# Optimization experiments

Measured on AMD Instinct MI355X. Metric: run time of the kernel, lower is better.

Reference implementation:

```python
import jax, jax.numpy as jnp
import numpy as np

EMA_DECAY = 0.9

K, B, D, d = 16, 2048, 1024, 64


def setup_inputs() -> dict:
    key = jax.random.key(0)
    k1, k2 = jax.random.split(key)
    x = jax.random.normal(k1, (B, D), dtype=jnp.float32)
    # subspace bases, scaled like orthonormal-ish columns
    Us = jax.random.normal(k2, (K, D, d), dtype=jnp.float32) / np.sqrt(D)
    c_mean = jnp.ones((K,), dtype=jnp.float32) / K
    return {"x": x, "Us": Us, "c_mean": c_mean}


def reference(x, Us, c_mean):
    # encode: per-subspace projection coefficients z = Us^T x  -> (k, B, d)
    z = jnp.einsum("bD,kDd->kbd", x, Us)
    # decode: x_ = z @ Us^T  -> (k, B, D)
    x_ = jnp.einsum("kbd,kDd->kbD", z, Us)
    # per-(sample, subspace) squared reconstruction loss -> (B, k)
    losses = jnp.sum((x[None, :, :] - x_) ** 2, axis=2).T
    # hard assignment: one-hot of argmin over subspaces (detached in original)
    assign_obj = jax.lax.stop_gradient(losses)
    minidx = jnp.argmin(assign_obj, axis=1)  # (B,)
    c = jax.nn.one_hot(minidx, K, dtype=losses.dtype)  # (B, k)
    # EMA cluster-usage statistics
    batch_c_mean = jnp.mean(c, axis=0)  # (k,)
    c_mean_new = EMA_DECAY * c_mean + (1.0 - EMA_DECAY) * batch_c_mean
    # objective: mean over batch of assigned losses, summed over clusters
    loss_k = jnp.mean(c * losses, axis=0)  # (k,)
    obj = jnp.sum(loss_k)
    return x_, c, c_mean_new, obj
```

## Files before the change

kernel.cpp:

```cpp
#include <hip/hip_runtime.h>

#define Kk  16
#define Bb  2048
#define Dd  1024
#define dd_ 64
#define BT  64
#define CH  64
#define PAD 68

__global__ __launch_bounds__(256) void k_xnorm(const float* __restrict__ x,
                                               float* __restrict__ xnorm) {
    int lane = threadIdx.x & 63;
    int w    = threadIdx.x >> 6;
    int b    = blockIdx.x * 4 + w;
    const float* xr = x + (size_t)b * Dd;
    float s = 0.f;
#pragma unroll
    for (int seg = 0; seg < 4; ++seg) {
        float4 v = *reinterpret_cast<const float4*>(xr + seg * 256 + lane * 4);
        s = fmaf(v.x, v.x, s); s = fmaf(v.y, v.y, s);
        s = fmaf(v.z, v.z, s); s = fmaf(v.w, v.w, s);
    }
#pragma unroll
    for (int off = 32; off > 0; off >>= 1) s += __shfl_down(s, off, 64);
    if (lane == 0) xnorm[b] = s;
}

__global__ __launch_bounds__(256) void k_fused(const float* __restrict__ x,
                                               const float* __restrict__ Us,
                                               float* __restrict__ xhat,
                                               float* __restrict__ znorm,
                                               float* __restrict__ hatnorm) {
    __shared__ float buf0[CH][PAD];
    __shared__ float buf1[CH][PAD];
    __shared__ float z_lds[dd_][PAD];
    __shared__ float hat_lds[BT];

    int t  = threadIdx.x;
    int tx = t & 15;
    int ty = t >> 4;

    int bid = blockIdx.x;
    int sw  = (bid & 7) * 64 + (bid >> 3);
    int k   = sw >> 5;
    int b0  = (sw & 31) * BT;

    const float* __restrict__ xk  = x  + (size_t)b0 * Dd;
    const float* __restrict__ Usk = Us + (size_t)k * Dd * dd_;

    if (t < BT) hat_lds[t] = 0.f;

    float acc[4][4];
#pragma unroll
    for (int i = 0; i < 4; ++i)
#pragma unroll
        for (int j = 0; j < 4; ++j) acc[i][j] = 0.f;

    for (int Dc = 0; Dc < Dd; Dc += CH) {
        __syncthreads();
#pragma unroll
        for (int rr = 0; rr < 4; ++rr) {
            int row = rr * 16 + ty;
            float4 v = *reinterpret_cast<const float4*>(
                xk + (size_t)row * Dd + Dc + tx * 4);
            buf0[tx * 4 + 0][row] = v.x;
            buf0[tx * 4 + 1][row] = v.y;
            buf0[tx * 4 + 2][row] = v.z;
            buf0[tx * 4 + 3][row] = v.w;
            float4 u = *reinterpret_cast<const float4*>(
                Usk + (size_t)(Dc + row) * dd_ + tx * 4);
            *reinterpret_cast<float4*>(&buf1[row][tx * 4]) = u;
        }
        __syncthreads();
#pragma unroll 8
        for (int kk = 0; kk < CH; ++kk) {
            float4 av = *reinterpret_cast<const float4*>(&buf0[kk][tx * 4]);
            float4 bv = *reinterpret_cast<const float4*>(&buf1[kk][ty * 4]);
            float a_[4] = {av.x, av.y, av.z, av.w};
            float b_[4] = {bv.x, bv.y, bv.z, bv.w};
#pragma unroll
            for (int i = 0; i < 4; ++i)
#pragma unroll
                for (int j = 0; j < 4; ++j)
                    acc[i][j] = fmaf(a_[i], b_[j], acc[i][j]);
        }
    }

#pragma unroll
    for (int i = 0; i < 4; ++i)
#pragma unroll
        for (int j = 0; j < 4; ++j)
            z_lds[ty * 4 + j][tx * 4 + i] = acc[i][j];
    __syncthreads();

    if (t < BT) {
        float s = 0.f;
#pragma unroll 8
        for (int dc = 0; dc < dd_; ++dc) {
            float zv = z_lds[dc][t];
            s = fmaf(zv, zv, s);
        }
        znorm[k * Bb + b0 + t] = s;
    }

    float hat[4] = {0.f, 0.f, 0.f, 0.f};
    for (int Dc = 0; Dc < Dd; Dc += CH) {
        __syncthreads();
#pragma unroll
        for (int rr = 0; rr < 4; ++rr) {
            int row = rr * 16 + ty;
            float4 u = *reinterpret_cast<const float4*>(
                Usk + (size_t)(Dc + row) * dd_ + tx * 4);
            buf0[tx * 4 + 0][row] = u.x;
            buf0[tx * 4 + 1][row] = u.y;
            buf0[tx * 4 + 2][row] = u.z;
            buf0[tx * 4 + 3][row] = u.w;
        }
        __syncthreads();

        float dacc[4][4];
#pragma unroll
        for (int i = 0; i < 4; ++i)
#pragma unroll
            for (int j = 0; j < 4; ++j) dacc[i][j] = 0.f;

#pragma unroll 8
        for (int kk = 0; kk < dd_; ++kk) {
            float4 av = *reinterpret_cast<const float4*>(&z_lds[kk][ty * 4]);
            float4 bv = *reinterpret_cast<const float4*>(&buf0[kk][tx * 4]);
            float a_[4] = {av.x, av.y, av.z, av.w};
            float b_[4] = {bv.x, bv.y, bv.z, bv.w};
#pragma unroll
            for (int i = 0; i < 4; ++i)
#pragma unroll
                for (int j = 0; j < 4; ++j)
                    dacc[i][j] = fmaf(a_[i], b_[j], dacc[i][j]);
        }

#pragma unroll
        for (int i = 0; i < 4; ++i) {
            float4 o = make_float4(dacc[i][0], dacc[i][1], dacc[i][2], dacc[i][3]);
            *reinterpret_cast<float4*>(
                xhat + ((size_t)(k * Bb + b0 + ty * 4 + i)) * Dd + Dc + tx * 4) = o;
            hat[i] = fmaf(o.x, o.x, hat[i]);
            hat[i] = fmaf(o.y, o.y, hat[i]);
            hat[i] = fmaf(o.z, o.z, hat[i]);
            hat[i] = fmaf(o.w, o.w, hat[i]);
        }
    }

    __syncthreads();
#pragma unroll
    for (int i = 0; i < 4; ++i) atomicAdd(&hat_lds[ty * 4 + i], hat[i]);
    __syncthreads();
    if (t < BT) hatnorm[k * Bb + b0 + t] = hat_lds[t];
}

__global__ __launch_bounds__(128) void k_assign(const float* __restrict__ znorm,
                                                const float* __restrict__ hatnorm,
                                                const float* __restrict__ xnorm,
                                                float* __restrict__ c,
                                                float* __restrict__ cnt_g,
                                                float* __restrict__ obj_g) {
    __shared__ float cnt[Kk];
    __shared__ float objacc;
    int t = threadIdx.x;
    int b = blockIdx.x * 128 + t;
    if (t < Kk) cnt[t] = 0.f;
    if (t == 0) objacc = 0.f;
    __syncthreads();

    float xn   = xnorm[b];
    float best = 3.4e38f;
    int   bi   = 0;
#pragma unroll
    for (int k = 0; k < Kk; ++k) {
        float l = xn - 2.f * znorm[k * Bb + b] + hatnorm[k * Bb + b];
        if (l < best) { best = l; bi = k; }
    }
#pragma unroll
    for (int j = 0; j < 4; ++j) {
        float4 o;
        o.x = (bi == j * 4 + 0) ? 1.f : 0.f;
        o.y = (bi == j * 4 + 1) ? 1.f : 0.f;
        o.z = (bi == j * 4 + 2) ? 1.f : 0.f;
        o.w = (bi == j * 4 + 3) ? 1.f : 0.f;
        *reinterpret_cast<float4*>(&c[(size_t)b * Kk + j * 4]) = o;
    }
    atomicAdd(&cnt[bi], 1.f);

    float lobj = best;
#pragma unroll
    for (int off = 32; off > 0; off >>= 1) lobj += __shfl_down(lobj, off, 64);
    if ((t & 63) == 0) atomicAdd(&objacc, lobj);
    __syncthreads();

    if (t < Kk) atomicAdd(&cnt_g[t], cnt[t]);
    if (t == 0) atomicAdd(obj_g, objacc);
}

__global__ __launch_bounds__(64) void k_epilogue(const float* __restrict__ cnt_g,
                                                 const float* __restrict__ obj_g,
                                                 const float* __restrict__ c_mean,
                                                 float* __restrict__ c_mean_new,
                                                 float* __restrict__ obj) {
    int t = threadIdx.x;
    if (t < Kk) c_mean_new[t] = 0.9f * c_mean[t] + 0.1f * (cnt_g[t] * (1.f / Bb));
    if (t == 0) obj[0] = obj_g[0] * (1.f / Bb);
}

extern "C" void kernel_launch(void* const* d_in, const int* in_sizes, int n_in,
                              void* d_out, int out_size, void* d_ws, size_t ws_size,
                              hipStream_t stream) {
    const float* x      = (const float*)d_in[0];
    const float* Us     = (const float*)d_in[1];
    const float* c_mean = (const float*)d_in[2];

    float* out        = (float*)d_out;
    float* xhat       = out;
    float* c          = out + (size_t)Kk * Bb * Dd;
    float* c_mean_new = c + (size_t)Bb * Kk;
    float* obj        = c_mean_new + Kk;

    float* ws      = (float*)d_ws;
    float* znorm   = ws;
    float* hatnorm = znorm + (size_t)Kk * Bb;
    float* xnorm   = hatnorm + (size_t)Kk * Bb;
    float* cnt_g   = xnorm + Bb;
    float* obj_g   = cnt_g + Kk;

    hipMemsetAsync(cnt_g, 0, (Kk + 1) * sizeof(float), stream);

    k_xnorm   <<<Bb / 4, 256, 0, stream>>>(x, xnorm);
    k_fused   <<<Kk * (Bb / BT), 256, 0, stream>>>(x, Us, xhat, znorm, hatnorm);
    k_assign  <<<Bb / 128, 128, 0, stream>>>(znorm, hatnorm, xnorm, c, cnt_g, obj_g);
    k_epilogue<<<1, 64, 0, stream>>>(cnt_g, obj_g, c_mean, c_mean_new, obj);
}
```

Baseline: 273.9 us.

## Register-prefetch next chunk, XOR-swizzle LDS, fold xnorm into assign, drop memset

The encode and decode loops now load the next chunk from global memory into registers while computing on the current one, then write it to LDS after a barrier. The transposed LDS buffer uses an XOR swizzle instead of padding to avoid bank conflicts. The z-norm is computed from the accumulators with LDS atomics, and only a combined hat-minus-2z term is written out. The separate xnorm kernel and the memset are removed: x norms are computed inside the assign kernel, which now writes per-block partials that a final kernel sums. This cuts launches, but the assign stage now runs on only 8 blocks that each read 256 rows of x serially.

```diff
diff --git a/kernel.cpp b/kernel.cpp
--- a/kernel.cpp
+++ b/kernel.cpp
@@ -6,34 +6,67 @@
 #define dd_ 64
 #define BT  64
 #define CH  64
-#define PAD 68
-
-__global__ __launch_bounds__(256) void k_xnorm(const float* __restrict__ x,
-                                               float* __restrict__ xnorm) {
-    int lane = threadIdx.x & 63;
-    int w    = threadIdx.x >> 6;
-    int b    = blockIdx.x * 4 + w;
-    const float* xr = x + (size_t)b * Dd;
-    float s = 0.f;
-#pragma unroll
-    for (int seg = 0; seg < 4; ++seg) {
-        float4 v = *reinterpret_cast<const float4*>(xr + seg * 256 + lane * 4);
-        s = fmaf(v.x, v.x, s); s = fmaf(v.y, v.y, s);
-        s = fmaf(v.z, v.z, s); s = fmaf(v.w, v.w, s);
-    }
-#pragma unroll
-    for (int off = 32; off > 0; off >>= 1) s += __shfl_down(s, off, 64);
-    if (lane == 0) xnorm[b] = s;
+#define NCH (Dd / CH)
+
+__device__ __forceinline__ int swz(int c) { return ((c >> 2) & 7) << 2; }
+
+__device__ __forceinline__ void enc_load(const float* __restrict__ xk,
+                                         const float* __restrict__ Usk,
+                                         int Dc, int tx, int ty,
+                                         float4 nx[4], float4 nu[4]) {
+#pragma unroll
+    for (int rr = 0; rr < 4; ++rr) {
+        int row = rr * 16 + ty;
+        nx[rr] = *reinterpret_cast<const float4*>(xk + (size_t)row * Dd + Dc + tx * 4);
+        nu[rr] = *reinterpret_cast<const float4*>(Usk + (size_t)(Dc + row) * dd_ + tx * 4);
+    }
+}
+
+__device__ __forceinline__ void enc_store(float (*bufT)[64], float (*bufS)[64],
+                                          int tx, int ty,
+                                          const float4 nx[4], const float4 nu[4]) {
+    int sx = (tx & 7) << 2;
+#pragma unroll
+    for (int rr = 0; rr < 4; ++rr) {
+        int row = rr * 16 + ty;
+        bufT[tx * 4 + 0][row ^ sx] = nx[rr].x;
+        bufT[tx * 4 + 1][row ^ sx] = nx[rr].y;
+        bufT[tx * 4 + 2][row ^ sx] = nx[rr].z;
+        bufT[tx * 4 + 3][row ^ sx] = nx[rr].w;
+        *reinterpret_cast<float4*>(&bufS[row][tx * 4]) = nu[rr];
+    }
+}
+
+__device__ __forceinline__ void dec_load(const float* __restrict__ Usk,
+                                         int Dc, int tx, int ty, float4 nU[4]) {
+#pragma unroll
+    for (int rr = 0; rr < 4; ++rr) {
+        int row = rr * 16 + ty;
+        nU[rr] = *reinterpret_cast<const float4*>(Usk + (size_t)(Dc + row) * dd_ + tx * 4);
+    }
+}
+
+__device__ __forceinline__ void dec_store(float (*bufT)[64], int tx, int ty,
+                                          const float4 nU[4]) {
+    int sx = (tx & 7) << 2;
+#pragma unroll
+    for (int rr = 0; rr < 4; ++rr) {
+        int row = rr * 16 + ty;
+        bufT[tx * 4 + 0][row ^ sx] = nU[rr].x;
+        bufT[tx * 4 + 1][row ^ sx] = nU[rr].y;
+        bufT[tx * 4 + 2][row ^ sx] = nU[rr].z;
+        bufT[tx * 4 + 3][row ^ sx] = nU[rr].w;
+    }
 }
 
 __global__ __launch_bounds__(256) void k_fused(const float* __restrict__ x,
                                                const float* __restrict__ Us,
                                                float* __restrict__ xhat,
-                                               float* __restrict__ znorm,
-                                               float* __restrict__ hatnorm) {
-    __shared__ float buf0[CH][PAD];
-    __shared__ float buf1[CH][PAD];
-    __shared__ float z_lds[dd_][PAD];
+                                               float* __restrict__ lterm) {
+    __shared__ float bufT[CH][64];
+    __shared__ float bufS[CH][64];
+    __shared__ float z_lds[dd_][68];
+    __shared__ float zn_lds[BT];
     __shared__ float hat_lds[BT];
 
     int t  = threadIdx.x;
@@ -48,7 +81,7 @@
     const float* __restrict__ xk  = x  + (size_t)b0 * Dd;
     const float* __restrict__ Usk = Us + (size_t)k * Dd * dd_;
 
-    if (t < BT) hat_lds[t] = 0.f;
+    if (t < BT) { zn_lds[t] = 0.f; hat_lds[t] = 0.f; }
 
     float acc[4][4];
 #pragma unroll
@@ -56,26 +89,19 @@
 #pragma unroll
         for (int j = 0; j < 4; ++j) acc[i][j] = 0.f;
 
-    for (int Dc = 0; Dc < Dd; Dc += CH) {
-        __syncthreads();
-#pragma unroll
-        for (int rr = 0; rr < 4; ++rr) {
-            int row = rr * 16 + ty;
-            float4 v = *reinterpret_cast<const float4*>(
-                xk + (size_t)row * Dd + Dc + tx * 4);
-            buf0[tx * 4 + 0][row] = v.x;
-            buf0[tx * 4 + 1][row] = v.y;
-            buf0[tx * 4 + 2][row] = v.z;
-            buf0[tx * 4 + 3][row] = v.w;
-            float4 u = *reinterpret_cast<const float4*>(
-                Usk + (size_t)(Dc + row) * dd_ + tx * 4);
-            *reinterpret_cast<float4*>(&buf1[row][tx * 4]) = u;
-        }
-        __syncthreads();
+    float4 nx[4], nu[4];
+    enc_load(xk, Usk, 0, tx, ty, nx, nu);
+    enc_store(bufT, bufS, tx, ty, nx, nu);
+    __syncthreads();
+
+    for (int ch = 0; ch < NCH; ++ch) {
+        bool more = (ch + 1 < NCH);
+        if (more) enc_load(xk, Usk, (ch + 1) * CH, tx, ty, nx, nu);
+
 #pragma unroll 8
         for (int kk = 0; kk < CH; ++kk) {
-            float4 av = *reinterpret_cast<const float4*>(&buf0[kk][tx * 4]);
-            float4 bv = *reinterpret_cast<const float4*>(&buf1[kk][ty * 4]);
+            float4 av = *reinterpret_cast<const float4*>(&bufT[kk][(tx * 4) ^ swz(kk)]);
+            float4 bv = *reinterpret_cast<const float4*>(&bufS[kk][ty * 4]);
             float a_[4] = {av.x, av.y, av.z, av.w};
             float b_[4] = {bv.x, bv.y, bv.z, bv.w};
 #pragma unroll
@@ -84,39 +110,32 @@
                 for (int j = 0; j < 4; ++j)
                     acc[i][j] = fmaf(a_[i], b_[j], acc[i][j]);
         }
-    }
-
-#pragma unroll
-    for (int i = 0; i < 4; ++i)
-#pragma unroll
-        for (int j = 0; j < 4; ++j)
+        __syncthreads();
+        if (more) { enc_store(bufT, bufS, tx, ty, nx, nu); __syncthreads(); }
+    }
+
+#pragma unroll
+    for (int i = 0; i < 4; ++i) {
+        float pz = 0.f;
+#pragma unroll
+        for (int j = 0; j < 4; ++j) {
             z_lds[ty * 4 + j][tx * 4 + i] = acc[i][j];
-    __syncthreads();
-
-    if (t < BT) {
-        float s = 0.f;
-#pragma unroll 8
-        for (int dc = 0; dc < dd_; ++dc) {
-            float zv = z_lds[dc][t];
-            s = fmaf(zv, zv, s);
-        }
-        znorm[k * Bb + b0 + t] = s;
-    }
+            pz = fmaf(acc[i][j], acc[i][j], pz);
+        }
+        atomicAdd(&zn_lds[tx * 4 + i], pz);
+    }
+    __syncthreads();
 
     float hat[4] = {0.f, 0.f, 0.f, 0.f};
-    for (int Dc = 0; Dc < Dd; Dc += CH) {
-        __syncthreads();
-#pragma unroll
-        for (int rr = 0; rr < 4; ++rr) {
-            int row = rr * 16 + ty;
-            float4 u = *reinterpret_cast<const float4*>(
-                Usk + (size_t)(Dc + row) * dd_ + tx * 4);
-            buf0[tx * 4 + 0][row] = u.x;
-            buf0[tx * 4 + 1][row] = u.y;
-            buf0[tx * 4 + 2][row] = u.z;
-            buf0[tx * 4 + 3][row] = u.w;
-        }
-        __syncthreads();
+    float4 nU[4];
+    dec_load(Usk, 0, tx, ty, nU);
+    dec_store(bufT, tx, ty, nU);
+    __syncthreads();
+
+    for (int ch = 0; ch < NCH; ++ch) {
+        bool more = (ch + 1 < NCH);
+        int  Dc   = ch * CH;
+        if (more) dec_load(Usk, Dc + CH, tx, ty, nU);
 
         float dacc[4][4];
 #pragma unroll
@@ -127,7 +146,7 @@
 #pragma unroll 8
         for (int kk = 0; kk < dd_; ++kk) {
             float4 av = *reinterpret_cast<const float4*>(&z_lds[kk][ty * 4]);
-            float4 bv = *reinterpret_cast<const float4*>(&buf0[kk][tx * 4]);
+            float4 bv = *reinterpret_cast<const float4*>(&bufT[kk][(tx * 4) ^ swz(kk)]);
             float a_[4] = {av.x, av.y, av.z, av.w};
             float b_[4] = {bv.x, bv.y, bv.z, bv.w};
 #pragma unroll
@@ -141,41 +160,61 @@
         for (int i = 0; i < 4; ++i) {
             float4 o = make_float4(dacc[i][0], dacc[i][1], dacc[i][2], dacc[i][3]);
             *reinterpret_cast<float4*>(
-                xhat + ((size_t)(k * Bb + b0 + ty * 4 + i)) * Dd + Dc + tx * 4) = o;
+                xhat + (size_t)(k * Bb + b0 + ty * 4 + i) * Dd + Dc + tx * 4) = o;
             hat[i] = fmaf(o.x, o.x, hat[i]);
             hat[i] = fmaf(o.y, o.y, hat[i]);
             hat[i] = fmaf(o.z, o.z, hat[i]);
             hat[i] = fmaf(o.w, o.w, hat[i]);
         }
-    }
-
-    __syncthreads();
+        __syncthreads();
+        if (more) { dec_store(bufT, tx, ty, nU); __syncthreads(); }
+    }
+
 #pragma unroll
     for (int i = 0; i < 4; ++i) atomicAdd(&hat_lds[ty * 4 + i], hat[i]);
     __syncthreads();
-    if (t < BT) hatnorm[k * Bb + b0 + t] = hat_lds[t];
-}
-
-__global__ __launch_bounds__(128) void k_assign(const float* __restrict__ znorm,
-                                                const float* __restrict__ hatnorm,
-                                                const float* __restrict__ xnorm,
+    if (t < BT) lterm[k * Bb + b0 + t] = hat_lds[t] - 2.f * zn_lds[t];
+}
+
+__global__ __launch_bounds__(256) void k_assign(const float* __restrict__ x,
+                                                const float* __restrict__ lterm,
                                                 float* __restrict__ c,
-                                                float* __restrict__ cnt_g,
-                                                float* __restrict__ obj_g) {
+                                                float* __restrict__ cnt_part,
+                                                float* __restrict__ obj_part) {
+    __shared__ float xn_lds[256];
     __shared__ float cnt[Kk];
     __shared__ float objacc;
-    int t = threadIdx.x;
-    int b = blockIdx.x * 128 + t;
+    int t    = threadIdx.x;
+    int lane = t & 63;
+    int w    = t >> 6;
+    int bbase = blockIdx.x * 256;
+
     if (t < Kk) cnt[t] = 0.f;
     if (t == 0) objacc = 0.f;
-    __syncthreads();
-
-    float xn   = xnorm[b];
+
+    for (int r = 0; r < 64; ++r) {
+        int bl = w * 64 + r;
+        const float* xr = x + (size_t)(bbase + bl) * Dd;
+        float s = 0.f;
+#pragma unroll
+        for (int seg = 0; seg < 4; ++seg) {
+            float4 v = *reinterpret_cast<const float4*>(xr + seg * 256 + lane * 4);
+            s = fmaf(v.x, v.x, s); s = fmaf(v.y, v.y, s);
+            s = fmaf(v.z, v.z, s); s = fmaf(v.w, v.w, s);
+        }
+#pragma unroll
+        for (int off = 32; off > 0; off >>= 1) s += __shfl_down(s, off, 64);
+        if (lane == 0) xn_lds[bl] = s;
+    }
+    __syncthreads();
+
+    int b = bbase + t;
+    float xn = xn_lds[t];
     float best = 3.4e38f;
     int   bi   = 0;
 #pragma unroll
     for (int k = 0; k < Kk; ++k) {
-        float l = xn - 2.f * znorm[k * Bb + b] + hatnorm[k * Bb + b];
+        float l = xn + lterm[k * Bb + b];
         if (l < best) { best = l; bi = k; }
     }
 #pragma unroll
@@ -192,21 +231,31 @@
     float lobj = best;
 #pragma unroll
     for (int off = 32; off > 0; off >>= 1) lobj += __shfl_down(lobj, off, 64);
-    if ((t & 63) == 0) atomicAdd(&objacc, lobj);
-    __syncthreads();
-
-    if (t < Kk) atomicAdd(&cnt_g[t], cnt[t]);
-    if (t == 0) atomicAdd(obj_g, objacc);
-}
-
-__global__ __launch_bounds__(64) void k_epilogue(const float* __restrict__ cnt_g,
-                                                 const float* __restrict__ obj_g,
-                                                 const float* __restrict__ c_mean,
-                                                 float* __restrict__ c_mean_new,
-                                                 float* __restrict__ obj) {
+    if (lane == 0) atomicAdd(&objacc, lobj);
+    __syncthreads();
+
+    if (t < Kk) cnt_part[blockIdx.x * Kk + t] = cnt[t];
+    if (t == 0) obj_part[blockIdx.x] = objacc;
+}
+
+__global__ __launch_bounds__(64) void k_final(const float* __restrict__ cnt_part,
+                                              const float* __restrict__ obj_part,
+                                              const float* __restrict__ c_mean,
+                                              float* __restrict__ c_mean_new,
+                                              float* __restrict__ obj) {
     int t = threadIdx.x;
-    if (t < Kk) c_mean_new[t] = 0.9f * c_mean[t] + 0.1f * (cnt_g[t] * (1.f / Bb));
-    if (t == 0) obj[0] = obj_g[0] * (1.f / Bb);
+    if (t < Kk) {
+        float s = 0.f;
+#pragma unroll
+        for (int p = 0; p < 8; ++p) s += cnt_part[p * Kk + t];
+        c_mean_new[t] = 0.9f * c_mean[t] + 0.1f * (s * (1.f / Bb));
+    }
+    if (t == 0) {
+        float s = 0.f;
+#pragma unroll
+        for (int p = 0; p < 8; ++p) s += obj_part[p];
+        obj[0] = s * (1.f / Bb);
+    }
 }
 
 extern "C" void kernel_launch(void* const* d_in, const int* in_sizes, int n_in,
@@ -222,17 +271,12 @@
     float* c_mean_new = c + (size_t)Bb * Kk;
     float* obj        = c_mean_new + Kk;
 
-    float* ws      = (float*)d_ws;
-    float* znorm   = ws;
-    float* hatnorm = znorm + (size_t)Kk * Bb;
-    float* xnorm   = hatnorm + (size_t)Kk * Bb;
-    float* cnt_g   = xnorm + Bb;
-    float* obj_g   = cnt_g + Kk;
-
-    hipMemsetAsync(cnt_g, 0, (Kk + 1) * sizeof(float), stream);
-
-    k_xnorm   <<<Bb / 4, 256, 0, stream>>>(x, xnorm);
-    k_fused   <<<Kk * (Bb / BT), 256, 0, stream>>>(x, Us, xhat, znorm, hatnorm);
-    k_assign  <<<Bb / 128, 128, 0, stream>>>(znorm, hatnorm, xnorm, c, cnt_g, obj_g);
-    k_epilogue<<<1, 64, 0, stream>>>(cnt_g, obj_g, c_mean, c_mean_new, obj);
-}
+    float* ws       = (float*)d_ws;
+    float* lterm    = ws;
+    float* cnt_part = lterm + (size_t)Kk * Bb;
+    float* obj_part = cnt_part + 8 * Kk;
+
+    k_fused <<<Kk * (Bb / BT), 256, 0, stream>>>(x, Us, xhat, lterm);
+    k_assign<<<Bb / 256, 256, 0, stream>>>(x, lterm, c, cnt_part, obj_part);
+    k_final <<<1, 64, 0, stream>>>(cnt_part, obj_part, c_mean, c_mean_new, obj);
+}
```

New measurement: 296.3 us. +8.2%, slower.
